# Kernel optimization log

Measured on AMD Instinct MI355X. Metric: run time of the kernel, lower is better.

## Reference

```python
import jax, jax.numpy as jnp
import numpy as np

N = 16384

def setup_inputs() -> dict:
    key = jax.random.key(0)
    k1, k2, k3 = jax.random.split(key, 3)
    hazard_pred = jax.random.normal(k1, (N, 1), dtype=jnp.float32)
    durations = jax.random.uniform(k2, (N,), dtype=jnp.float32)
    events = jax.random.uniform(k3, (N,), dtype=jnp.float32)
    return {"hazard_pred": hazard_pred, "durations": durations, "events": events}

def reference(hazard_pred, durations, events):
    theta = hazard_pred.reshape(-1)                      # [n]
    # risk-set mask: R[i, j] = durations[j] >= durations[i]
    R = (durations[None, :] >= durations[:, None]).astype(theta.dtype)  # [n, n]
    # sum_j exp(theta_j) * R[i, j]  -> fused masked row-sum (single GEMV)
    risk_sum = R @ jnp.exp(theta)                        # [n]
    loss_cox = -jnp.mean((theta - jnp.log(risk_sum)) * events)
    return loss_cox
```

## Files before the change

kernel.cpp:

```cpp
#include <hip/hip_runtime.h>
#include <math.h>

#define NB    2048
#define BLK   256
#define SCANT 1024


__device__ __forceinline__ int bucket_of(float d) {
    int b = (int)(d * (float)NB);
    return min(max(b, 0), NB - 1);
}

__global__ __launch_bounds__(BLK)
void zero_kernel(int* __restrict__ ws_i) {
    int i = blockIdx.x * BLK + threadIdx.x;
    if (i < 4098) ws_i[i] = 0;
}

__global__ __launch_bounds__(BLK)
void stats_kernel(const float* __restrict__ hazard,
                  const float* __restrict__ durations,
                  float* __restrict__ sumExp, int* __restrict__ cnt, int n) {
    int j = blockIdx.x * BLK + threadIdx.x;
    if (j >= n) return;
    float d = durations[j];
    float e = expf(hazard[j]);
    int b = bucket_of(d);
    atomicAdd(&sumExp[b], e);
    atomicAdd(&cnt[b], 1);
}

__global__ __launch_bounds__(SCANT)
void scan_kernel(const float* __restrict__ sumExp, const int* __restrict__ cnt,
                 int* __restrict__ offsets, int* __restrict__ cursor,
                 float* __restrict__ suffixGT) {
    __shared__ float fa[NB], fb[NB];
    __shared__ int   ia[NB], ib[NB];
    const int tid = threadIdx.x;

    #pragma unroll
    for (int k = 0; k < NB / SCANT; ++k) {
        int idx = tid + k * SCANT;
        fa[idx] = sumExp[NB - 1 - idx];
        ia[idx] = cnt[idx];
    }
    __syncthreads();

    bool pa = true;
    for (int d = 1; d < NB; d <<= 1) {
        #pragma unroll
        for (int k = 0; k < NB / SCANT; ++k) {
            int idx = tid + k * SCANT;
            float fsrc = pa ? fa[idx] : fb[idx];
            int   isrc = pa ? ia[idx] : ib[idx];
            float fadd = (idx >= d) ? (pa ? fa[idx - d] : fb[idx - d]) : 0.0f;
            int   iadd = (idx >= d) ? (pa ? ia[idx - d] : ib[idx - d]) : 0;
            if (pa) { fb[idx] = fsrc + fadd; ib[idx] = isrc + iadd; }
            else    { fa[idx] = fsrc + fadd; ia[idx] = isrc + iadd; }
        }
        __syncthreads();
        pa = !pa;
    }
    #pragma unroll
    for (int k = 0; k < NB / SCANT; ++k) {
        int idx = tid + k * SCANT;
        int iexcl = (idx > 0) ? (pa ? ia[idx - 1] : ib[idx - 1]) : 0;
        offsets[idx] = iexcl;
        cursor[idx]  = iexcl;
        suffixGT[idx] = (idx + 1 < NB) ? (pa ? fa[NB - 2 - idx] : fb[NB - 2 - idx]) : 0.0f;
    }
}

__global__ __launch_bounds__(BLK)
void scatter_kernel(const float* __restrict__ hazard,
                    const float* __restrict__ durations,
                    const int* __restrict__ offsets,
                    int* __restrict__ cursor,
                    float2* __restrict__ sorted, int n) {
    int j = blockIdx.x * BLK + threadIdx.x;
    if (j >= n) return;
    float d = durations[j];
    float e = expf(hazard[j]);
    int b = bucket_of(d);
    int pos = atomicAdd(&cursor[b], 1);
    sorted[pos] = make_float2(d, e);
}

__global__ __launch_bounds__(BLK)
void loss_kernel(const float* __restrict__ hazard,
                 const float* __restrict__ durations,
                 const float* __restrict__ events,
                 const int* __restrict__ offsets, const int* __restrict__ cnt,
                 const float* __restrict__ suffixGT,
                 const float2* __restrict__ sorted,
                 float* __restrict__ wsum, int* __restrict__ done,
                 float* __restrict__ out, int n) {
    const int i = blockIdx.x * BLK + threadIdx.x;
    float d = durations[i];
    int b = bucket_of(d);
    float s = suffixGT[b];
    int off = offsets[b], c = cnt[b];
    for (int k = 0; k < c; ++k) {
        float2 v = sorted[off + k];
        s += (v.x >= d) ? v.y : 0.0f;
    }
    float local = (hazard[i] - logf(s)) * events[i];

    #pragma unroll
    for (int o = 32; o > 0; o >>= 1)
        local += __shfl_down(local, o, 64);

    __shared__ float wpart[BLK / 64];
    if ((threadIdx.x & 63) == 0) wpart[threadIdx.x >> 6] = local;
    __syncthreads();
    if (threadIdx.x == 0) {
        float t = 0.0f;
        #pragma unroll
        for (int w = 0; w < BLK / 64; ++w) t += wpart[w];
        atomicAdd(wsum, t);
        __threadfence();
        int ticket = atomicAdd(done, 1);
        if (ticket == (int)gridDim.x - 1) {
            float tot = atomicAdd(wsum, 0.0f);
            out[0] = -tot / (float)n;
        }
    }
}

extern "C" void kernel_launch(void* const* d_in, const int* in_sizes, int n_in,
                              void* d_out, int out_size, void* d_ws, size_t ws_size,
                              hipStream_t stream) {
    const float* hazard    = (const float*)d_in[0];
    const float* durations = (const float*)d_in[1];
    const float* events    = (const float*)d_in[2];
    float* out = (float*)d_out;
    const int n = in_sizes[1];

    char* ws = (char*)d_ws;
    float*  sumExp   = (float*)(ws + 0);
    int*    cnt      = (int*)  (ws + 8192);
    float*  wsum     = (float*)(ws + 16384);
    int*    done     = (int*)  (ws + 16388);
    int*    offsets  = (int*)  (ws + 16640);
    int*    cursor   = (int*)  (ws + 24832);
    float*  suffixGT = (float*)(ws + 33024);
    float2* sorted   = (float2*)(ws + 41216);

    const int nblk = (n + BLK - 1) / BLK;

    zero_kernel   <<<17, BLK, 0, stream>>>((int*)ws);
    stats_kernel  <<<nblk, BLK, 0, stream>>>(hazard, durations, sumExp, cnt, n);
    scan_kernel   <<<1, SCANT, 0, stream>>>(sumExp, cnt, offsets, cursor, suffixGT);
    scatter_kernel<<<nblk, BLK, 0, stream>>>(hazard, durations, offsets, cursor, sorted, n);
    loss_kernel   <<<nblk, BLK, 0, stream>>>(hazard, durations, events, offsets, cnt,
                                             suffixGT, sorted, wsum, done, out, n);
}
```

Baseline: 77.63 us.

## Fuse bucket-sort Cox loss pipeline into a single-workgroup kernel

```diff
diff --git a/kernel.cpp b/kernel.cpp
--- a/kernel.cpp
+++ b/kernel.cpp
@@ -2,8 +2,8 @@
 #include <math.h>
 
 #define NB    2048
-#define BLK   256
-#define SCANT 1024
+#define BLK   1024
+#define ELEMS 16
 
 
 __device__ __forceinline__ int bucket_of(float d) {
@@ -12,45 +12,59 @@
 }
 
 __global__ __launch_bounds__(BLK)
-void zero_kernel(int* __restrict__ ws_i) {
-    int i = blockIdx.x * BLK + threadIdx.x;
-    if (i < 4098) ws_i[i] = 0;
-}
-
-__global__ __launch_bounds__(BLK)
-void stats_kernel(const float* __restrict__ hazard,
-                  const float* __restrict__ durations,
-                  float* __restrict__ sumExp, int* __restrict__ cnt, int n) {
-    int j = blockIdx.x * BLK + threadIdx.x;
-    if (j >= n) return;
-    float d = durations[j];
-    float e = expf(hazard[j]);
-    int b = bucket_of(d);
-    atomicAdd(&sumExp[b], e);
-    atomicAdd(&cnt[b], 1);
-}
-
-__global__ __launch_bounds__(SCANT)
-void scan_kernel(const float* __restrict__ sumExp, const int* __restrict__ cnt,
-                 int* __restrict__ offsets, int* __restrict__ cursor,
-                 float* __restrict__ suffixGT) {
+void fused_cox_kernel(const float* __restrict__ hazard,
+                      const float* __restrict__ durations,
+                      const float* __restrict__ events,
+                      float2* __restrict__ sorted,
+                      float* __restrict__ out, int n) {
+    __shared__ float sumExpH[NB];
+    __shared__ int   cntH[NB];
     __shared__ float fa[NB], fb[NB];
     __shared__ int   ia[NB], ib[NB];
+    __shared__ int   cursor[NB];
+    __shared__ float wpart[BLK / 64];
+
     const int tid = threadIdx.x;
 
     #pragma unroll
-    for (int k = 0; k < NB / SCANT; ++k) {
-        int idx = tid + k * SCANT;
-        fa[idx] = sumExp[NB - 1 - idx];
-        ia[idx] = cnt[idx];
+    for (int k = 0; k < NB / BLK; ++k) {
+        sumExpH[tid + k * BLK] = 0.0f;
+        cntH[tid + k * BLK]    = 0;
+    }
+    __syncthreads();
+
+    float dreg[ELEMS], ereg[ELEMS], hreg[ELEMS];
+    int   breg[ELEMS];
+    #pragma unroll
+    for (int k = 0; k < ELEMS; ++k) {
+        int i = tid + k * BLK;
+        if (i < n) {
+            float d = durations[i];
+            float h = hazard[i];
+            float e = expf(h);
+            int   b = bucket_of(d);
+            dreg[k] = d; hreg[k] = h; ereg[k] = e; breg[k] = b;
+            atomicAdd(&sumExpH[b], e);
+            atomicAdd(&cntH[b], 1);
+        } else {
+            breg[k] = -1;
+        }
+    }
+    __syncthreads();
+
+    #pragma unroll
+    for (int k = 0; k < NB / BLK; ++k) {
+        int idx = tid + k * BLK;
+        fa[idx] = sumExpH[NB - 1 - idx];
+        ia[idx] = cntH[idx];
     }
     __syncthreads();
 
     bool pa = true;
     for (int d = 1; d < NB; d <<= 1) {
         #pragma unroll
-        for (int k = 0; k < NB / SCANT; ++k) {
-            int idx = tid + k * SCANT;
+        for (int k = 0; k < NB / BLK; ++k) {
+            int idx = tid + k * BLK;
             float fsrc = pa ? fa[idx] : fb[idx];
             int   isrc = pa ? ia[idx] : ib[idx];
             float fadd = (idx >= d) ? (pa ? fa[idx - d] : fb[idx - d]) : 0.0f;
@@ -61,69 +75,60 @@
         __syncthreads();
         pa = !pa;
     }
+    if (pa) {
+        #pragma unroll
+        for (int k = 0; k < NB / BLK; ++k) {
+            int idx = tid + k * BLK;
+            fb[idx] = fa[idx];
+            ib[idx] = ia[idx];
+        }
+        __syncthreads();
+    }
+
     #pragma unroll
-    for (int k = 0; k < NB / SCANT; ++k) {
-        int idx = tid + k * SCANT;
-        int iexcl = (idx > 0) ? (pa ? ia[idx - 1] : ib[idx - 1]) : 0;
-        offsets[idx] = iexcl;
-        cursor[idx]  = iexcl;
-        suffixGT[idx] = (idx + 1 < NB) ? (pa ? fa[NB - 2 - idx] : fb[NB - 2 - idx]) : 0.0f;
+    for (int k = 0; k < NB / BLK; ++k) {
+        int idx = tid + k * BLK;
+        cursor[idx] = (idx > 0) ? ib[idx - 1] : 0;
     }
-}
+    __syncthreads();
 
-__global__ __launch_bounds__(BLK)
-void scatter_kernel(const float* __restrict__ hazard,
-                    const float* __restrict__ durations,
-                    const int* __restrict__ offsets,
-                    int* __restrict__ cursor,
-                    float2* __restrict__ sorted, int n) {
-    int j = blockIdx.x * BLK + threadIdx.x;
-    if (j >= n) return;
-    float d = durations[j];
-    float e = expf(hazard[j]);
-    int b = bucket_of(d);
-    int pos = atomicAdd(&cursor[b], 1);
-    sorted[pos] = make_float2(d, e);
-}
+    #pragma unroll
+    for (int k = 0; k < ELEMS; ++k) {
+        if (breg[k] >= 0) {
+            int pos = atomicAdd(&cursor[breg[k]], 1);
+            sorted[pos] = make_float2(dreg[k], ereg[k]);
+        }
+    }
+    __syncthreads();
 
-__global__ __launch_bounds__(BLK)
-void loss_kernel(const float* __restrict__ hazard,
-                 const float* __restrict__ durations,
-                 const float* __restrict__ events,
-                 const int* __restrict__ offsets, const int* __restrict__ cnt,
-                 const float* __restrict__ suffixGT,
-                 const float2* __restrict__ sorted,
-                 float* __restrict__ wsum, int* __restrict__ done,
-                 float* __restrict__ out, int n) {
-    const int i = blockIdx.x * BLK + threadIdx.x;
-    float d = durations[i];
-    int b = bucket_of(d);
-    float s = suffixGT[b];
-    int off = offsets[b], c = cnt[b];
-    for (int k = 0; k < c; ++k) {
-        float2 v = sorted[off + k];
-        s += (v.x >= d) ? v.y : 0.0f;
+    float local = 0.0f;
+    #pragma unroll
+    for (int k = 0; k < ELEMS; ++k) {
+        int i = tid + k * BLK;
+        if (i < n) {
+            int   b = breg[k];
+            float d = dreg[k];
+            float s = (b + 1 < NB) ? fb[NB - 2 - b] : 0.0f;
+            int c   = cntH[b];
+            int off = cursor[b] - c;
+            for (int t = 0; t < c; ++t) {
+                float2 v = sorted[off + t];
+                s += (v.x >= d) ? v.y : 0.0f;
+            }
+            local += (hreg[k] - logf(s)) * events[i];
+        }
     }
-    float local = (hazard[i] - logf(s)) * events[i];
 
     #pragma unroll
     for (int o = 32; o > 0; o >>= 1)
         local += __shfl_down(local, o, 64);
-
-    __shared__ float wpart[BLK / 64];
-    if ((threadIdx.x & 63) == 0) wpart[threadIdx.x >> 6] = local;
+    if ((tid & 63) == 0) wpart[tid >> 6] = local;
     __syncthreads();
-    if (threadIdx.x == 0) {
-        float t = 0.0f;
+    if (tid == 0) {
+        float tot = 0.0f;
         #pragma unroll
-        for (int w = 0; w < BLK / 64; ++w) t += wpart[w];
-        atomicAdd(wsum, t);
-        __threadfence();
-        int ticket = atomicAdd(done, 1);
-        if (ticket == (int)gridDim.x - 1) {
-            float tot = atomicAdd(wsum, 0.0f);
-            out[0] = -tot / (float)n;
-        }
+        for (int w = 0; w < BLK / 64; ++w) tot += wpart[w];
+        out[0] = -tot / (float)n;
     }
 }
 
@@ -136,22 +141,7 @@
     float* out = (float*)d_out;
     const int n = in_sizes[1];
 
-    char* ws = (char*)d_ws;
-    float*  sumExp   = (float*)(ws + 0);
-    int*    cnt      = (int*)  (ws + 8192);
-    float*  wsum     = (float*)(ws + 16384);
-    int*    done     = (int*)  (ws + 16388);
-    int*    offsets  = (int*)  (ws + 16640);
-    int*    cursor   = (int*)  (ws + 24832);
-    float*  suffixGT = (float*)(ws + 33024);
-    float2* sorted   = (float2*)(ws + 41216);
+    float2* sorted = (float2*)d_ws;
 
-    const int nblk = (n + BLK - 1) / BLK;
-
-    zero_kernel   <<<17, BLK, 0, stream>>>((int*)ws);
-    stats_kernel  <<<nblk, BLK, 0, stream>>>(hazard, durations, sumExp, cnt, n);
-    scan_kernel   <<<1, SCANT, 0, stream>>>(sumExp, cnt, offsets, cursor, suffixGT);
-    scatter_kernel<<<nblk, BLK, 0, stream>>>(hazard, durations, offsets, cursor, sorted, n);
-    loss_kernel   <<<nblk, BLK, 0, stream>>>(hazard, durations, events, offsets, cnt,
-                                             suffixGT, sorted, wsum, done, out, n);
+    fused_cox_kernel<<<1, BLK, 0, stream>>>(hazard, durations, events, sorted, out, n);
 }
```

After: 167.9 us. 116% more time.
